# Optimization experiments

Measured on AMD Instinct MI355X. Metric: run time of the kernel, lower is better.

## Reference

```python
import jax, jax.numpy as jnp
import numpy as np

RADIUS = 2  # half window; original kernel truncates the spatial Gaussian at ~2.5*sigma


def setup_inputs() -> dict:
    key = jax.random.key(0)
    input_img = jax.random.normal(key, (2, 1, 128, 128, 128), dtype=jnp.float32)
    return {
        "input_img": input_img,
        "sigma_x": jnp.float32(1.0),
        "sigma_y": jnp.float32(1.0),
        "sigma_z": jnp.float32(1.0),
        "color_sigma": jnp.float32(0.5),
    }


def reference(input_img, sigma_x, sigma_y, sigma_z, color_sigma):
    # 3D bilateral filter: out(i) = sum_k w_spatial(k) * w_range(x_i, x_k) * x_k / sum_k w
    R = RADIUS
    pad = [(0, 0), (0, 0), (R, R), (R, R), (R, R)]
    xp = jnp.pad(input_img, pad)                       # zero-padded volume
    mp = jnp.pad(jnp.ones_like(input_img), pad)        # validity mask (out-of-bounds taps excluded)

    offs = np.array([(dx, dy, dz)
                     for dx in range(-R, R + 1)
                     for dy in range(-R, R + 1)
                     for dz in range(-R, R + 1)], dtype=np.int32)  # (K,3), K=125
    d2 = jnp.asarray(offs.astype(np.float32) ** 2)     # squared offsets (K,3)
    w_sp = jnp.exp(-(d2[:, 0] / (2.0 * sigma_x ** 2)
                     + d2[:, 1] / (2.0 * sigma_y ** 2)
                     + d2[:, 2] / (2.0 * sigma_z ** 2)))  # (K,)
    starts = jnp.asarray(offs + R)                     # slice starts into the padded volume

    inv_2cs2 = 1.0 / (2.0 * color_sigma ** 2)
    shape = input_img.shape

    def body(carry, inp):
        num, den = carry
        start, ws = inp
        s = jnp.concatenate([jnp.zeros(2, jnp.int32), start])
        xk = jax.lax.dynamic_slice(xp, s, shape)       # shifted neighbor volume
        mk = jax.lax.dynamic_slice(mp, s, shape)
        w = ws * mk * jnp.exp(-(input_img - xk) ** 2 * inv_2cs2)
        return (num + w * xk, den + w), None

    zero = jnp.zeros_like(input_img)
    (num, den), _ = jax.lax.scan(body, (zero, zero), (starts, w_sp))
    return num / den
```

## Files before the change

### kernel.cpp

```cpp
#include <hip/hip_runtime.h>
#include <hip/hip_bf16.h>


#define RADIUS 2
#define N 128
#define TX 16
#define TY 8
#define TZ 8
#define PITCH (TX + 2 * RADIUS)
#define LYD (TY + 2 * RADIUS)
#define LZD (TZ + 2 * RADIUS)
#define LDS_SIZE (PITCH * LYD * LZD)

#define LOG2E 1.4426950408889634f
#define BIG 1.0e18f
#define EXP2_SCALE 8388608.0f
#define EXP2_BIAS 1065353216.0f

__global__ __launch_bounds__(256, 4) void bilateral3d_kernel(
    const float* __restrict__ in, const float* __restrict__ p_sx,
    const float* __restrict__ p_sy, const float* __restrict__ p_sz,
    const float* __restrict__ p_cs, float* __restrict__ out) {
  __shared__ float s[LDS_SIZE];

  const int tid = threadIdx.x;
  const int x0 = blockIdx.x * TX;
  const int y0 = blockIdx.y * TY;
  const int zb = blockIdx.z;
  const int z0 = (zb & 15) * TZ;
  const int b = zb >> 4;

  const float* vol = in + (size_t)b * (N * N * N);

  for (int i = tid; i < LDS_SIZE; i += 256) {
    int lx = i % PITCH;
    int t = i / PITCH;
    int ly = t % LYD;
    int lz = t / LYD;
    int gx = x0 + lx - RADIUS;
    int gy = y0 + ly - RADIUS;
    int gz = z0 + lz - RADIUS;
    float v = BIG;
    if ((unsigned)gx < N && (unsigned)gy < N && (unsigned)gz < N)
      v = vol[((size_t)gz * N + gy) * N + gx];
    s[i] = v;
  }
  __syncthreads();

  const int tx = tid & 3;
  const int ty = (tid >> 2) & 7;
  const int tz = tid >> 5;

  const float sxv = p_sx[0], syv = p_sy[0], szv = p_sz[0], csv = p_cs[0];
  const float AX2 = EXP2_SCALE * LOG2E / (2.0f * sxv * sxv);
  const float AY2 = EXP2_SCALE * LOG2E / (2.0f * syv * syv);
  const float AZ2 = EXP2_SCALE * LOG2E / (2.0f * szv * szv);
  const float NAC2 = -(EXP2_SCALE * LOG2E) / (2.0f * csv * csv);
  const float AX2_4 = 4.0f * AX2;

  const int xw = 4 * tx;

  const int cbase = ((tz + RADIUS) * LYD + (ty + RADIUS)) * PITCH + xw;
  const float4 CA = *(const float4*)&s[cbase];
  const float4 CB = *(const float4*)&s[cbase + 4];
  const float xc0 = CA.z, xc1 = CA.w, xc2 = CB.x, xc3 = CB.y;

  float n0 = 0, n1 = 0, n2 = 0, n3 = 0;
  float e0 = 0, e1 = 0, e2 = 0, e3 = 0;

#define TAP(XC, FV, CC, NN, DD)                          \
  {                                                      \
    float _d = (XC) - (FV);                              \
    float _f = fmaf(_d * _d, NAC2, (CC));                \
    unsigned _q;                                         \
    asm("v_cvt_u32_f32 %0, %1" : "=v"(_q) : "v"(_f));    \
    float _w = __uint_as_float(_q);                      \
    DD += _w;                                            \
    NN = fmaf(_w, (FV), NN);                             \
  }

#pragma unroll 1
  for (int dz = -RADIUS; dz <= RADIUS; ++dz) {
    const float pz2 = AZ2 * (float)(dz * dz);
    const int zrow = (tz + RADIUS + dz) * LYD;
#pragma unroll
    for (int dy = -RADIUS; dy <= RADIUS; ++dy) {
      const float cc0 = EXP2_BIAS - (pz2 + AY2 * (float)(dy * dy));
      const float cm1 = cc0 - AX2;
      const float cm4 = cc0 - AX2_4;
      const int rb = (zrow + (ty + RADIUS + dy)) * PITCH + xw;
      const float4 A = *(const float4*)&s[rb];
      const float4 B = *(const float4*)&s[rb + 4];
      const float f0 = A.x, f1 = A.y, f2 = A.z, f3 = A.w;
      const float f4 = B.x, f5 = B.y, f6 = B.z, f7 = B.w;

      TAP(xc0, f0, cm4, n0, e0)
      TAP(xc1, f1, cm4, n1, e1)
      TAP(xc2, f2, cm4, n2, e2)
      TAP(xc3, f3, cm4, n3, e3)
      TAP(xc0, f1, cm1, n0, e0)
      TAP(xc1, f2, cm1, n1, e1)
      TAP(xc2, f3, cm1, n2, e2)
      TAP(xc3, f4, cm1, n3, e3)
      TAP(xc0, f2, cc0, n0, e0)
      TAP(xc1, f3, cc0, n1, e1)
      TAP(xc2, f4, cc0, n2, e2)
      TAP(xc3, f5, cc0, n3, e3)
      TAP(xc0, f3, cm1, n0, e0)
      TAP(xc1, f4, cm1, n1, e1)
      TAP(xc2, f5, cm1, n2, e2)
      TAP(xc3, f6, cm1, n3, e3)
      TAP(xc0, f4, cm4, n0, e0)
      TAP(xc1, f5, cm4, n1, e1)
      TAP(xc2, f6, cm4, n2, e2)
      TAP(xc3, f7, cm4, n3, e3)
    }
  }

  float4 r;
  r.x = n0 / e0;
  r.y = n1 / e1;
  r.z = n2 / e2;
  r.w = n3 / e3;

  const int gz = z0 + tz, gy = y0 + ty;
  *(float4*)&out[(((size_t)b * N + gz) * N + gy) * N + (x0 + xw)] = r;
}

extern "C" void kernel_launch(void* const* d_in, const int* in_sizes, int n_in,
                              void* d_out, int out_size, void* d_ws, size_t ws_size,
                              hipStream_t stream) {
  const float* in = (const float*)d_in[0];
  const float* sx = (const float*)d_in[1];
  const float* sy = (const float*)d_in[2];
  const float* sz = (const float*)d_in[3];
  const float* cs = (const float*)d_in[4];
  float* out = (float*)d_out;

  dim3 grid(N / TX, N / TY, (N / TZ) * 2);
  bilateral3d_kernel<<<grid, 256, 0, stream>>>(in, sx, sy, sz, cs, out);
}
```

Baseline: 146.5 us.

## Compute eight x-outputs per thread and software-pipeline LDS row loads

Each thread now produces eight consecutive x outputs instead of four, so the tile widens to 32 in x and the shared-memory halo is amortized over more outputs. Each 12-float neighbor row is reused across eight centers, which cuts LDS reads per tap. The next row's loads are issued before the current row's taps are computed, hiding LDS latency. Register use rises, so launch bounds drop to two blocks per CU, reducing occupancy.

```diff
diff --git a/kernel.cpp b/kernel.cpp
--- a/kernel.cpp
+++ b/kernel.cpp
@@ -4,9 +4,10 @@
 
 #define RADIUS 2
 #define N 128
-#define TX 16
+#define TX 32
 #define TY 8
 #define TZ 8
+#define VPT 8
 #define PITCH (TX + 2 * RADIUS)
 #define LYD (TY + 2 * RADIUS)
 #define LZD (TZ + 2 * RADIUS)
@@ -17,7 +18,7 @@
 #define EXP2_SCALE 8388608.0f
 #define EXP2_BIAS 1065353216.0f
 
-__global__ __launch_bounds__(256, 4) void bilateral3d_kernel(
+__global__ __launch_bounds__(256, 2) void bilateral3d_kernel(
     const float* __restrict__ in, const float* __restrict__ p_sx,
     const float* __restrict__ p_sy, const float* __restrict__ p_sz,
     const float* __restrict__ p_cs, float* __restrict__ out) {
@@ -58,15 +59,18 @@
   const float NAC2 = -(EXP2_SCALE * LOG2E) / (2.0f * csv * csv);
   const float AX2_4 = 4.0f * AX2;
 
-  const int xw = 4 * tx;
+  const int xw = VPT * tx;
+  const int yb = ty + RADIUS;
 
-  const int cbase = ((tz + RADIUS) * LYD + (ty + RADIUS)) * PITCH + xw;
-  const float4 CA = *(const float4*)&s[cbase];
-  const float4 CB = *(const float4*)&s[cbase + 4];
-  const float xc0 = CA.z, xc1 = CA.w, xc2 = CB.x, xc3 = CB.y;
+  const int cbase = ((tz + RADIUS) * LYD + yb) * PITCH + xw;
+  const float4 K0 = *(const float4*)&s[cbase];
+  const float4 K1 = *(const float4*)&s[cbase + 4];
+  const float4 K2 = *(const float4*)&s[cbase + 8];
+  const float xc0 = K0.z, xc1 = K0.w, xc2 = K1.x, xc3 = K1.y;
+  const float xc4 = K1.z, xc5 = K1.w, xc6 = K2.x, xc7 = K2.y;
 
-  float n0 = 0, n1 = 0, n2 = 0, n3 = 0;
-  float e0 = 0, e1 = 0, e2 = 0, e3 = 0;
+  float n0 = 0, n1 = 0, n2 = 0, n3 = 0, n4 = 0, n5 = 0, n6 = 0, n7 = 0;
+  float e0 = 0, e1 = 0, e2 = 0, e3 = 0, e4 = 0, e5 = 0, e6 = 0, e7 = 0;
 
 #define TAP(XC, FV, CC, NN, DD)                          \
   {                                                      \
@@ -79,52 +83,69 @@
     NN = fmaf(_w, (FV), NN);                             \
   }
 
+#define TAPS5(I, F0, F1, F2, F3, F4, NN, DD) \
+  TAP(xc##I, F0, cm4, NN, DD)                \
+  TAP(xc##I, F1, cm1, NN, DD)                \
+  TAP(xc##I, F2, cc0, NN, DD)                \
+  TAP(xc##I, F3, cm1, NN, DD)                \
+  TAP(xc##I, F4, cm4, NN, DD)
+
+  int rb = (tz * LYD + (yb - 2)) * PITCH + xw;
+  float4 A = *(const float4*)&s[rb];
+  float4 Bv = *(const float4*)&s[rb + 4];
+  float4 C = *(const float4*)&s[rb + 8];
+
 #pragma unroll 1
   for (int dz = -RADIUS; dz <= RADIUS; ++dz) {
     const float pz2 = AZ2 * (float)(dz * dz);
-    const int zrow = (tz + RADIUS + dz) * LYD;
-#pragma unroll
-    for (int dy = -RADIUS; dy <= RADIUS; ++dy) {
-      const float cc0 = EXP2_BIAS - (pz2 + AY2 * (float)(dy * dy));
-      const float cm1 = cc0 - AX2;
-      const float cm4 = cc0 - AX2_4;
-      const int rb = (zrow + (ty + RADIUS + dy)) * PITCH + xw;
-      const float4 A = *(const float4*)&s[rb];
-      const float4 B = *(const float4*)&s[rb + 4];
-      const float f0 = A.x, f1 = A.y, f2 = A.z, f3 = A.w;
-      const float f4 = B.x, f5 = B.y, f6 = B.z, f7 = B.w;
+    const int zi = tz + RADIUS + dz;
 
-      TAP(xc0, f0, cm4, n0, e0)
-      TAP(xc1, f1, cm4, n1, e1)
-      TAP(xc2, f2, cm4, n2, e2)
-      TAP(xc3, f3, cm4, n3, e3)
-      TAP(xc0, f1, cm1, n0, e0)
-      TAP(xc1, f2, cm1, n1, e1)
-      TAP(xc2, f3, cm1, n2, e2)
-      TAP(xc3, f4, cm1, n3, e3)
-      TAP(xc0, f2, cc0, n0, e0)
-      TAP(xc1, f3, cc0, n1, e1)
-      TAP(xc2, f4, cc0, n2, e2)
-      TAP(xc3, f5, cc0, n3, e3)
-      TAP(xc0, f3, cm1, n0, e0)
-      TAP(xc1, f4, cm1, n1, e1)
-      TAP(xc2, f5, cm1, n2, e2)
-      TAP(xc3, f6, cm1, n3, e3)
-      TAP(xc0, f4, cm4, n0, e0)
-      TAP(xc1, f5, cm4, n1, e1)
-      TAP(xc2, f6, cm4, n2, e2)
-      TAP(xc3, f7, cm4, n3, e3)
+#define ROW(DY)                                                              \
+    {                                                                        \
+      int _rn;                                                               \
+      if ((DY) < 2) {                                                        \
+        _rn = (zi * LYD + (yb + (DY) + 1)) * PITCH + xw;                     \
+      } else {                                                               \
+        int _zn = zi + 1;                                                    \
+        _zn = _zn > (LZD - 1) ? (LZD - 1) : _zn;                             \
+        _rn = (_zn * LYD + (yb - 2)) * PITCH + xw;                           \
+      }                                                                      \
+      float4 A2 = *(const float4*)&s[_rn];                                   \
+      float4 B2 = *(const float4*)&s[_rn + 4];                               \
+      float4 C2 = *(const float4*)&s[_rn + 8];                               \
+      const float cc0 = EXP2_BIAS - (pz2 + AY2 * (float)((DY) * (DY)));      \
+      const float cm1 = cc0 - AX2;                                           \
+      const float cm4 = cc0 - AX2_4;                                         \
+      const float f0 = A.x, f1 = A.y, f2 = A.z, f3 = A.w;                    \
+      const float f4 = Bv.x, f5 = Bv.y, f6 = Bv.z, f7 = Bv.w;                \
+      const float f8 = C.x, f9 = C.y, f10 = C.z, f11 = C.w;                  \
+      TAPS5(0, f0, f1, f2, f3, f4, n0, e0)                                   \
+      TAPS5(1, f1, f2, f3, f4, f5, n1, e1)                                   \
+      TAPS5(2, f2, f3, f4, f5, f6, n2, e2)                                   \
+      TAPS5(3, f3, f4, f5, f6, f7, n3, e3)                                   \
+      TAPS5(4, f4, f5, f6, f7, f8, n4, e4)                                   \
+      TAPS5(5, f5, f6, f7, f8, f9, n5, e5)                                   \
+      TAPS5(6, f6, f7, f8, f9, f10, n6, e6)                                  \
+      TAPS5(7, f7, f8, f9, f10, f11, n7, e7)                                 \
+      A = A2; Bv = B2; C = C2;                                               \
     }
+
+    ROW(-2)
+    ROW(-1)
+    ROW(0)
+    ROW(1)
+    ROW(2)
+#undef ROW
   }
 
-  float4 r;
-  r.x = n0 / e0;
-  r.y = n1 / e1;
-  r.z = n2 / e2;
-  r.w = n3 / e3;
+  float4 r0, r1;
+  r0.x = n0 / e0; r0.y = n1 / e1; r0.z = n2 / e2; r0.w = n3 / e3;
+  r1.x = n4 / e4; r1.y = n5 / e5; r1.z = n6 / e6; r1.w = n7 / e7;
 
   const int gz = z0 + tz, gy = y0 + ty;
-  *(float4*)&out[(((size_t)b * N + gz) * N + gy) * N + (x0 + xw)] = r;
+  float* op = &out[(((size_t)b * N + gz) * N + gy) * N + (x0 + xw)];
+  *(float4*)op = r0;
+  *(float4*)(op + 4) = r1;
 }
 
 extern "C" void kernel_launch(void* const* d_in, const int* in_sizes, int n_in,
```

Result: slower. 158.4 us (+8.1%).

## Store LDS tile as scaled fp16 and evaluate taps with packed f16 mix ops

Applied to the files above, without the earlier changes.

The halo tile is now stored in LDS as fp16, pre-scaled by the square root of the range constant. The taps use v_pk_add_f16 for paired differences and v_fma_mix_f32 for the squared-distance exponent and the accumulation. The exp2 bit trick moves to an fp16-based bias (BASE16), is clamped with fmax, and the final division is corrected by the scale. This halves LDS footprint and traffic and cuts VALU work per tap; launch bounds rise to 6 waves for occupancy, at the cost of fp16 precision in the differences and in the weights.

```diff
diff --git a/kernel.cpp b/kernel.cpp
--- a/kernel.cpp
+++ b/kernel.cpp
@@ -14,14 +14,15 @@
 
 #define LOG2E 1.4426950408889634f
 #define BIG 1.0e18f
-#define EXP2_SCALE 8388608.0f
-#define EXP2_BIAS 1065353216.0f
+#define MAGIC 8388608.0f
+#define BASE16 8403968.0f
+#define SENT 60000.0f
 
-__global__ __launch_bounds__(256, 4) void bilateral3d_kernel(
+__global__ __launch_bounds__(256, 6) void bilateral3d_kernel(
     const float* __restrict__ in, const float* __restrict__ p_sx,
     const float* __restrict__ p_sy, const float* __restrict__ p_sz,
     const float* __restrict__ p_cs, float* __restrict__ out) {
-  __shared__ float s[LDS_SIZE];
+  __shared__ _Float16 h[LDS_SIZE];
 
   const int tid = threadIdx.x;
   const int x0 = blockIdx.x * TX;
@@ -29,6 +30,14 @@
   const int zb = blockIdx.z;
   const int z0 = (zb & 15) * TZ;
   const int b = zb >> 4;
+
+  const float sxv = p_sx[0], syv = p_sy[0], szv = p_sz[0], csv = p_cs[0];
+  const float K10 = 1024.0f * LOG2E;
+  const float AX2 = K10 / (2.0f * sxv * sxv);
+  const float AY2 = K10 / (2.0f * syv * syv);
+  const float AZ2 = K10 / (2.0f * szv * szv);
+  const float AX2_4 = 4.0f * AX2;
+  const float sR = __builtin_sqrtf(K10 / (2.0f * csv * csv));
 
   const float* vol = in + (size_t)b * (N * N * N);
 
@@ -43,7 +52,7 @@
     float v = BIG;
     if ((unsigned)gx < N && (unsigned)gy < N && (unsigned)gz < N)
       v = vol[((size_t)gz * N + gy) * N + gx];
-    s[i] = v;
+    h[i] = (_Float16)__builtin_fminf(v * sR, SENT);
   }
   __syncthreads();
 
@@ -51,32 +60,62 @@
   const int ty = (tid >> 2) & 7;
   const int tz = tid >> 5;
 
-  const float sxv = p_sx[0], syv = p_sy[0], szv = p_sz[0], csv = p_cs[0];
-  const float AX2 = EXP2_SCALE * LOG2E / (2.0f * sxv * sxv);
-  const float AY2 = EXP2_SCALE * LOG2E / (2.0f * syv * syv);
-  const float AZ2 = EXP2_SCALE * LOG2E / (2.0f * szv * szv);
-  const float NAC2 = -(EXP2_SCALE * LOG2E) / (2.0f * csv * csv);
-  const float AX2_4 = 4.0f * AX2;
-
   const int xw = 4 * tx;
+  const unsigned* hw = (const unsigned*)h;
 
   const int cbase = ((tz + RADIUS) * LYD + (ty + RADIUS)) * PITCH + xw;
-  const float4 CA = *(const float4*)&s[cbase];
-  const float4 CB = *(const float4*)&s[cbase + 4];
-  const float xc0 = CA.z, xc1 = CA.w, xc2 = CB.x, xc3 = CB.y;
+  const unsigned cw1 = hw[(cbase >> 1) + 1];
+  const unsigned cw2 = hw[(cbase >> 1) + 2];
+  const unsigned XS0 = __builtin_amdgcn_perm(cw1, cw1, 0x01000100);
+  const unsigned XS1 = __builtin_amdgcn_perm(cw1, cw1, 0x03020302);
+  const unsigned XS2 = __builtin_amdgcn_perm(cw2, cw2, 0x01000100);
+  const unsigned XS3 = __builtin_amdgcn_perm(cw2, cw2, 0x03020302);
 
   float n0 = 0, n1 = 0, n2 = 0, n3 = 0;
   float e0 = 0, e1 = 0, e2 = 0, e3 = 0;
 
-#define TAP(XC, FV, CC, NN, DD)                          \
-  {                                                      \
-    float _d = (XC) - (FV);                              \
-    float _f = fmaf(_d * _d, NAC2, (CC));                \
-    unsigned _q;                                         \
-    asm("v_cvt_u32_f32 %0, %1" : "=v"(_q) : "v"(_f));    \
-    float _w = __uint_as_float(_q);                      \
-    DD += _w;                                            \
-    NN = fmaf(_w, (FV), NN);                             \
+#define PKMIX(XS, GW, CL, CH, NN, DD)                                       \
+  {                                                                         \
+    unsigned _t;                                                            \
+    asm("v_pk_add_f16 %0, %1, %2 neg_lo:[0,1] neg_hi:[0,1]"                 \
+        : "=v"(_t) : "v"(XS), "v"(GW));                                     \
+    float _yl, _yh;                                                         \
+    asm("v_fma_mix_f32 %0, %1, -%1, %2 op_sel_hi:[1,1,0]"                   \
+        : "=v"(_yl) : "v"(_t), "v"(CL));                                    \
+    asm("v_fma_mix_f32 %0, %1, -%1, %2 op_sel:[1,1,0] op_sel_hi:[1,1,0]"    \
+        : "=v"(_yh) : "v"(_t), "v"(CH));                                    \
+    _yl = __builtin_fmaxf(_yl, MAGIC);                                      \
+    _yh = __builtin_fmaxf(_yh, MAGIC);                                      \
+    asm("v_fma_mix_f32 %0, %1, %2, %0 op_sel_hi:[1,1,0]"                    \
+        : "+v"(NN) : "v"(_yl), "v"(GW));                                    \
+    asm("v_fma_mix_f32 %0, %1, %2, %0 op_sel:[0,1,0] op_sel_hi:[1,1,0]"     \
+        : "+v"(NN) : "v"(_yh), "v"(GW));                                    \
+    asm("v_fma_mix_f32 %0, %1, 1.0, %0 op_sel_hi:[1,0,0]"                   \
+        : "+v"(DD) : "v"(_yl));                                             \
+    asm("v_fma_mix_f32 %0, %1, 1.0, %0 op_sel_hi:[1,0,0]"                   \
+        : "+v"(DD) : "v"(_yh));                                             \
+  }
+
+#define SC2MIX(XSAB, GP, CC, NA, DA, NB, DB)                                \
+  {                                                                         \
+    unsigned _t;                                                            \
+    asm("v_pk_add_f16 %0, %1, %2 neg_lo:[0,1] neg_hi:[0,1]"                 \
+        : "=v"(_t) : "v"(XSAB), "v"(GP));                                   \
+    float _yl, _yh;                                                         \
+    asm("v_fma_mix_f32 %0, %1, -%1, %2 op_sel_hi:[1,1,0]"                   \
+        : "=v"(_yl) : "v"(_t), "v"(CC));                                    \
+    asm("v_fma_mix_f32 %0, %1, -%1, %2 op_sel:[1,1,0] op_sel_hi:[1,1,0]"    \
+        : "=v"(_yh) : "v"(_t), "v"(CC));                                    \
+    _yl = __builtin_fmaxf(_yl, MAGIC);                                      \
+    _yh = __builtin_fmaxf(_yh, MAGIC);                                      \
+    asm("v_fma_mix_f32 %0, %1, %2, %0 op_sel_hi:[1,1,0]"                    \
+        : "+v"(NA) : "v"(_yl), "v"(GP));                                    \
+    asm("v_fma_mix_f32 %0, %1, %2, %0 op_sel:[0,1,0] op_sel_hi:[1,1,0]"     \
+        : "+v"(NB) : "v"(_yh), "v"(GP));                                    \
+    asm("v_fma_mix_f32 %0, %1, 1.0, %0 op_sel_hi:[1,0,0]"                   \
+        : "+v"(DA) : "v"(_yl));                                             \
+    asm("v_fma_mix_f32 %0, %1, 1.0, %0 op_sel_hi:[1,0,0]"                   \
+        : "+v"(DB) : "v"(_yh));                                             \
   }
 
 #pragma unroll 1
@@ -85,43 +124,41 @@
     const int zrow = (tz + RADIUS + dz) * LYD;
 #pragma unroll
     for (int dy = -RADIUS; dy <= RADIUS; ++dy) {
-      const float cc0 = EXP2_BIAS - (pz2 + AY2 * (float)(dy * dy));
+      const float cc0 = BASE16 - (pz2 + AY2 * (float)(dy * dy));
       const float cm1 = cc0 - AX2;
       const float cm4 = cc0 - AX2_4;
+
       const int rb = (zrow + (ty + RADIUS + dy)) * PITCH + xw;
-      const float4 A = *(const float4*)&s[rb];
-      const float4 B = *(const float4*)&s[rb + 4];
-      const float f0 = A.x, f1 = A.y, f2 = A.z, f3 = A.w;
-      const float f4 = B.x, f5 = B.y, f6 = B.z, f7 = B.w;
+      const int rb2 = rb >> 1;
+      const uint2 Wa = *(const uint2*)&hw[rb2];
+      const uint2 Wb = *(const uint2*)&hw[rb2 + 2];
+      const unsigned w0 = Wa.x, w1 = Wa.y, w2 = Wb.x, w3 = Wb.y;
 
-      TAP(xc0, f0, cm4, n0, e0)
-      TAP(xc1, f1, cm4, n1, e1)
-      TAP(xc2, f2, cm4, n2, e2)
-      TAP(xc3, f3, cm4, n3, e3)
-      TAP(xc0, f1, cm1, n0, e0)
-      TAP(xc1, f2, cm1, n1, e1)
-      TAP(xc2, f3, cm1, n2, e2)
-      TAP(xc3, f4, cm1, n3, e3)
-      TAP(xc0, f2, cc0, n0, e0)
-      TAP(xc1, f3, cc0, n1, e1)
-      TAP(xc2, f4, cc0, n2, e2)
-      TAP(xc3, f5, cc0, n3, e3)
-      TAP(xc0, f3, cm1, n0, e0)
-      TAP(xc1, f4, cm1, n1, e1)
-      TAP(xc2, f5, cm1, n2, e2)
-      TAP(xc3, f6, cm1, n3, e3)
-      TAP(xc0, f4, cm4, n0, e0)
-      TAP(xc1, f5, cm4, n1, e1)
-      TAP(xc2, f6, cm4, n2, e2)
-      TAP(xc3, f7, cm4, n3, e3)
+      PKMIX(XS0, w0, cm4, cm1, n0, e0)
+      PKMIX(XS0, w1, cc0, cm1, n0, e0)
+      PKMIX(XS1, w1, cm1, cc0, n1, e1)
+      PKMIX(XS1, w2, cm1, cm4, n1, e1)
+      PKMIX(XS2, w1, cm4, cm1, n2, e2)
+      PKMIX(XS2, w2, cc0, cm1, n2, e2)
+      PKMIX(XS3, w2, cm1, cc0, n3, e3)
+      PKMIX(XS3, w3, cm1, cm4, n3, e3)
+
+      {
+        const unsigned GP = __builtin_amdgcn_perm(w0, w2, 0x07060100);
+        SC2MIX(cw1, GP, cm4, n0, e0, n1, e1)
+      }
+      {
+        const unsigned GP = __builtin_amdgcn_perm(w1, w3, 0x07060100);
+        SC2MIX(cw2, GP, cm4, n2, e2, n3, e3)
+      }
     }
   }
 
   float4 r;
-  r.x = n0 / e0;
-  r.y = n1 / e1;
-  r.z = n2 / e2;
-  r.w = n3 / e3;
+  r.x = n0 / (e0 * sR);
+  r.y = n1 / (e1 * sR);
+  r.z = n2 / (e2 * sR);
+  r.w = n3 / (e3 * sR);
 
   const int gz = z0 + tz, gy = y0 + ty;
   *(float4*)&out[(((size_t)b * N + gz) * N + gy) * N + (x0 + xw)] = r;
```

After: 156.1 us. 6.5% more time.
